# Kernel tuning notes

Measured on AMD Instinct MI355X. Metric: run time of the kernel, lower is better.

## Reference

```python
import jax, jax.numpy as jnp
import numpy as np

B, N, L, H, D, IN = 512, 128, 10, 16, 8, 16
NT = B * N
E = NT * 16

def _lin(key, fan_in, shape):
    b = 1.0 / np.sqrt(fan_in)
    return jax.random.uniform(key, shape, jnp.float32, -b, b)

def setup_inputs() -> dict:
    key = jax.random.key(0)
    ks = jax.random.split(key, 12)
    x = jax.random.normal(ks[0], (NT, IN), jnp.float32)
    # within-graph random edges so to_dense_adj is well defined
    g = jax.random.randint(ks[1], (E,), 0, B)
    i = jax.random.randint(ks[2], (E,), 0, N)
    j = jax.random.randint(ks[3], (E,), 0, N)
    edge_index = jnp.stack([g * N + i, g * N + j]).astype(jnp.int32)
    return dict(
        x=x,
        gin_w1=_lin(ks[4], H, (2, L, H, H)),   # [ld/ud, layer, H, H]
        gin_b1=_lin(ks[5], H, (2, L, H)),
        gin_w2=_lin(ks[6], H, (2, L, H, H)),
        gin_b2=_lin(ks[7], H, (2, L, H)),
        mean_w=_lin(ks[8], H, (2, H, D)),
        mean_b=jnp.zeros((2, D), jnp.float32),
        std_w=_lin(ks[9], H, (2, H, D)),
        std_b=jnp.zeros((2, D), jnp.float32),
        edge_index=edge_index,
    )

def _encoder(x, w1, b1, w2, b2, mw, mb, sw, sb, src, dst):
    # PyG GIN stack: GINConv(MLP[Lin->ReLU->Lin]), eps=0, sum aggregation,
    # ReLU between layers (dropout = identity in eval mode).
    h = x
    for l in range(L):
        agg = jax.ops.segment_sum(h[src], dst, num_segments=NT)
        t = h + agg  # (1+eps)*x + sum_{j in N(i)} x_j with eps=0
        t = jnp.maximum(t @ w1[l] + b1[l], 0.0) @ w2[l] + b2[l]
        h = jnp.maximum(t, 0.0) if l < L - 1 else t
    mean = h @ mw + mb
    std = jax.nn.softplus(h @ sw + sb)
    return mean, std

def reference(x, gin_w1, gin_b1, gin_w2, gin_b2, mean_w, mean_b, std_w, std_b, edge_index):
    src, dst = edge_index[0], edge_index[1]
    enc = jax.vmap(_encoder, in_axes=(None, 0, 0, 0, 0, 0, 0, 0, 0, None, None))
    mean, std = enc(x, gin_w1, gin_b1, gin_w2, gin_b2,
                    mean_w, mean_b, std_w, std_b, src, dst)  # [2, NT, D]
    # reparameterized sample: eps ~ N(0,1) (prior.sample, detached)
    eps = jax.random.normal(jax.random.key(42), (2, NT, D), jnp.float32)
    z = mean + std * eps
    z_ld = z[0].reshape(B, N, D)
    z_ud = z[1].reshape(B, N, D)
    logits = jnp.einsum('bnd,bmd->bnm', z_ld, z_ud)  # per-graph inner-product decode
    dense_adj = jnp.zeros((B, N, N), jnp.float32).at[src // N, src % N, dst % N].add(1.0)
    n_pos = dense_adj.sum()
    posw = (B * N * N - n_pos) / n_pos
    # BCE-with-logits, pos_weight, reduction='sum'
    nll = jnp.sum(posw * dense_adj * jax.nn.softplus(-logits)
                  + (1.0 - dense_adj) * jax.nn.softplus(logits))
    # KL(N(mean,std) || N(0,1)), summed over both encoders
    kl = jnp.sum(-jnp.log(std) + 0.5 * (std * std + mean * mean) - 0.5)
    return nll, kl, jax.nn.sigmoid(logits), dense_adj
```

## Files before the change

kernel.cpp:

```cpp
#include <hip/hip_runtime.h>

#define B_    512
#define N_    128
#define L_    10
#define H_    16
#define D_    8
#define NT_   65536
#define E_    1048576
#define NNB_  8388608
#define CAP_  4096
#define CCAP_ 2816
#define HS_   20

__device__ __forceinline__ unsigned rotl32(unsigned v, int r){ return (v<<r)|(v>>(32-r)); }

__device__ __forceinline__ void threefry2x32(unsigned c0, unsigned c1, unsigned &o0, unsigned &o1){
  const unsigned ks0 = 0u, ks1 = 42u, ks2 = 0u ^ 42u ^ 0x1BD11BDAu;
  unsigned x0 = c0 + ks0, x1 = c1 + ks1;
#define TFR(r) { x0 += x1; x1 = rotl32(x1, r); x1 ^= x0; }
  TFR(13) TFR(15) TFR(26) TFR(6)   x0 += ks1; x1 += ks2 + 1u;
  TFR(17) TFR(29) TFR(16) TFR(24)  x0 += ks2; x1 += ks0 + 2u;
  TFR(13) TFR(15) TFR(26) TFR(6)   x0 += ks0; x1 += ks1 + 3u;
  TFR(17) TFR(29) TFR(16) TFR(24)  x0 += ks1; x1 += ks2 + 4u;
  TFR(13) TFR(15) TFR(26) TFR(6)   x0 += ks2; x1 += ks0 + 5u;
#undef TFR
  o0 = x0; o1 = x1;
}

__device__ __forceinline__ float erfinv_f(float x){
  float w = -log1pf(-x*x);
  float p;
  if (w < 5.0f) {
    w -= 2.5f;
    p = 2.81022636e-08f;
    p = fmaf(p, w, 3.43273939e-07f);
    p = fmaf(p, w, -3.5233877e-06f);
    p = fmaf(p, w, -4.39150654e-06f);
    p = fmaf(p, w, 0.00021858087f);
    p = fmaf(p, w, -0.00125372503f);
    p = fmaf(p, w, -0.00417768164f);
    p = fmaf(p, w, 0.246640727f);
    p = fmaf(p, w, 1.50140941f);
  } else {
    w = sqrtf(w) - 3.0f;
    p = -0.000200214257f;
    p = fmaf(p, w, 0.000100950558f);
    p = fmaf(p, w, 0.00134934322f);
    p = fmaf(p, w, -0.00367342844f);
    p = fmaf(p, w, 0.00573950773f);
    p = fmaf(p, w, -0.0076224613f);
    p = fmaf(p, w, 0.00943887047f);
    p = fmaf(p, w, 1.00167406f);
    p = fmaf(p, w, 2.83297682f);
  }
  return p * x;
}

__device__ __forceinline__ float softplus_f(float x){
  return fmaxf(x, 0.0f) + log1pf(expf(-fabsf(x)));
}

__device__ __forceinline__ void blockReduceAdd(double v, double* target){
  __shared__ double red[4];
  int lane = threadIdx.x & 63;
  int w    = threadIdx.x >> 6;
  #pragma unroll
  for(int off = 32; off > 0; off >>= 1) v += __shfl_down(v, off);
  if(lane == 0) red[w] = v;
  __syncthreads();
  if(threadIdx.x == 0){
    double s = red[0];
    int nw = (blockDim.x + 63) >> 6;
    for(int k = 1; k < nw; k++) s += red[k];
    atomicAdd(target, s);
  }
}

__global__ __launch_bounds__(256)
void k_bin(const int* __restrict__ ei, int* __restrict__ gcount,
           unsigned short* __restrict__ ebuf){
  __shared__ int cnt[512];
  __shared__ int gb[512];
  const int t = threadIdx.x;
  cnt[t] = 0; cnt[t + 256] = 0;
  __syncthreads();
  int kv[8];
  const int base = blockIdx.x * 2048;
  #pragma unroll
  for(int q = 0; q < 8; q++){
    int e = base + q*256 + t;
    int s = ei[e];
    int d = ei[E_ + e];
    int g = d >> 7;
    kv[q] = (g << 14) | ((s & 127) << 7) | (d & 127);
    atomicAdd(&cnt[g], 1);
  }
  __syncthreads();
  #pragma unroll
  for(int g = 0; g < 512; g += 256){
    int c = cnt[g + t];
    gb[g + t] = c ? atomicAdd(&gcount[g + t], c) : 0;
    cnt[g + t] = 0;
  }
  __syncthreads();
  #pragma unroll
  for(int q = 0; q < 8; q++){
    int g = kv[q] >> 14;
    int pos = atomicAdd(&cnt[g], 1);
    int idx = gb[g] + pos;
    if(idx < CAP_) ebuf[(size_t)g*CAP_ + idx] = (unsigned short)(kv[q] & 0x3FFF);
  }
}

__global__ __launch_bounds__(128)
void k_csr(const unsigned short* __restrict__ ebuf, const int* __restrict__ gcount,
           unsigned short* __restrict__ gcol, int* __restrict__ grow){
  __shared__ int cnt[128], off[128], sc[128];
  const int b = blockIdx.x, t = threadIdx.x;
  int ec = gcount[b]; if(ec > CAP_) ec = CAP_;
  const unsigned short* eb = ebuf + (size_t)b*CAP_;
  cnt[t] = 0;
  __syncthreads();
  for(int q = t; q < ec; q += 128) atomicAdd(&cnt[eb[q] & 127], 1);
  __syncthreads();
  int pdeg = (cnt[t] + 3) & ~3;
  sc[t] = pdeg;
  __syncthreads();
  for(int o = 1; o < 128; o <<= 1){
    int v = (t >= o) ? sc[t - o] : 0;
    __syncthreads();
    sc[t] += v;
    __syncthreads();
  }
  off[t] = sc[t] - pdeg;
  grow[b*129 + t] = off[t];
  if(t == 127) grow[b*129 + 128] = sc[127];
  cnt[t] = 0;
  __syncthreads();
  {
    uint4 s128; s128.x = s128.y = s128.z = s128.w = 0x00800080u;
    uint4* g4 = (uint4*)(gcol + (size_t)b*CCAP_);
    #pragma unroll
    for(int k = 0; k < 3; k++){ int q = t + 128*k; if(q < CCAP_/8) g4[q] = s128; }
  }
  __syncthreads();
  for(int q = t; q < ec; q += 128){
    int pk = eb[q];
    int d = pk & 127;
    int pos = atomicAdd(&cnt[d], 1);
    int idx = off[d] + pos;
    if(idx < CCAP_) gcol[(size_t)b*CCAP_ + idx] = (unsigned short)(pk >> 7);
  }
}

__global__ __launch_bounds__(256, 4)
void k_mega(const float* __restrict__ x, const unsigned short* __restrict__ gcol,
            const int* __restrict__ grow,
            const float* __restrict__ gw1, const float* __restrict__ gb1,
            const float* __restrict__ gw2, const float* __restrict__ gb2,
            const float* __restrict__ mw,  const float* __restrict__ mb,
            const float* __restrict__ sw,  const float* __restrict__ sb,
            float* __restrict__ z, double* acc){
  __shared__ __align__(16) float hh[2][129*HS_ + 4];
  __shared__ __align__(16) unsigned short col_l[CCAP_];
  const int b = blockIdx.x, e = blockIdx.y, t = threadIdx.x;
  const int i = t >> 1, p = t & 1;

  {
    const float4* x4 = (const float4*)x + (size_t)b*512;
    #pragma unroll
    for(int k = 0; k < 2; k++){
      int q = t + 256*k;
      float4 v = x4[q];
      *(float4*)&hh[0][(q >> 2)*HS_ + (q & 3)*4] = v;
    }
    if(t < 16){ hh[0][128*HS_ + t] = 0.0f; hh[1][128*HS_ + t] = 0.0f; }
  }
  {
    const uint4* gc4 = (const uint4*)(gcol + (size_t)b*CCAP_);
    uint4* cl4 = (uint4*)col_l;
    #pragma unroll
    for(int k = 0; k < 2; k++){ int q = t + 256*k; if(q < CCAP_/8) cl4[q] = gc4[q]; }
  }
  const int r0 = grow[b*129 + i], r1 = grow[b*129 + i + 1];
  __syncthreads();

  const float* w1g = gw1 + e*(L_*256);
  const float* w2g = gw2 + e*(L_*256);
  const float* b1g = gb1 + e*(L_*16);
  const float* b2g = gb2 + e*(L_*16);

  for(int l = 0; l < L_; l++){
    const float* hb = hh[l & 1];
    float*       hn = hh[(l + 1) & 1];
    float a[8];
    {
      const float4* hp = (const float4*)&hb[i*HS_ + p*8];
      float4 s0 = hp[0], s1 = hp[1];
      a[0]=s0.x; a[1]=s0.y; a[2]=s0.z; a[3]=s0.w;
      a[4]=s1.x; a[5]=s1.y; a[6]=s1.z; a[7]=s1.w;
    }
    for(int r = r0; r < r1; r += 4){
      ushort4 c4 = *(const ushort4*)&col_l[r];
      const float4* n0 = (const float4*)&hb[c4.x*HS_ + p*8];
      const float4* n1 = (const float4*)&hb[c4.y*HS_ + p*8];
      const float4* n2 = (const float4*)&hb[c4.z*HS_ + p*8];
      const float4* n3 = (const float4*)&hb[c4.w*HS_ + p*8];
      #pragma unroll
      for(int c = 0; c < 2; c++){
        float4 v0 = n0[c], v1 = n1[c], v2 = n2[c], v3 = n3[c];
        a[c*4+0] += v0.x + v1.x + v2.x + v3.x;
        a[c*4+1] += v0.y + v1.y + v2.y + v3.y;
        a[c*4+2] += v0.z + v1.z + v2.z + v3.z;
        a[c*4+3] += v0.w + v1.w + v2.w + v3.w;
      }
    }
    float ag[16];
    #pragma unroll
    for(int q = 0; q < 8; q++){
      float o = __shfl_xor(a[q], 1);
      ag[q]     = p ? o    : a[q];
      ag[q + 8] = p ? a[q] : o;
    }
    float u[16];
    #pragma unroll
    for(int j = 0; j < 16; j++){
      float s = b1g[l*16 + j];
      #pragma unroll
      for(int k = 0; k < 16; k++) s = fmaf(ag[k], w1g[l*256 + k*16 + j], s);
      u[j] = fmaxf(s, 0.0f);
    }
    float ov[16];
    #pragma unroll
    for(int c = 0; c < 16; c++){
      float s = b2g[l*16 + c];
      #pragma unroll
      for(int k = 0; k < 16; k++) s = fmaf(u[k], w2g[l*256 + k*16 + c], s);
      ov[c] = (l < L_-1) ? fmaxf(s, 0.0f) : s;
    }
    {
      float4* hw = (float4*)&hn[i*HS_ + p*8];
      hw[0] = make_float4(p ? ov[8]  : ov[0], p ? ov[9]  : ov[1],
                          p ? ov[10] : ov[2], p ? ov[11] : ov[3]);
      hw[1] = make_float4(p ? ov[12] : ov[4], p ? ov[13] : ov[5],
                          p ? ov[14] : ov[6], p ? ov[15] : ov[7]);
    }
    __syncthreads();
  }

  float hv[16];
  {
    const float4* hp = (const float4*)&hh[0][i*HS_];
    float4 a0 = hp[0], a1 = hp[1], a2 = hp[2], a3 = hp[3];
    hv[0]=a0.x; hv[1]=a0.y; hv[2]=a0.z; hv[3]=a0.w;
    hv[4]=a1.x; hv[5]=a1.y; hv[6]=a1.z; hv[7]=a1.w;
    hv[8]=a2.x; hv[9]=a2.y; hv[10]=a2.z; hv[11]=a2.w;
    hv[12]=a3.x; hv[13]=a3.y; hv[14]=a3.z; hv[15]=a3.w;
  }
  const float* mwg = mw + e*128 + p*4; const float* mbg = mb + e*8 + p*4;
  const float* swg = sw + e*128 + p*4; const float* sbg = sb + e*8 + p*4;
  double kll = 0.0;
  float zv[4];
  unsigned fbase = ((unsigned)e*NT_ + (unsigned)(b*128 + i))*8u + (unsigned)(p*4);
  float mmv[4], ssv[4];
  {
    float4 m4 = *(const float4*)mbg;
    float4 s4 = *(const float4*)sbg;
    mmv[0]=m4.x; mmv[1]=m4.y; mmv[2]=m4.z; mmv[3]=m4.w;
    ssv[0]=s4.x; ssv[1]=s4.y; ssv[2]=s4.z; ssv[3]=s4.w;
    #pragma unroll
    for(int k = 0; k < 16; k++){
      float4 mw4 = *(const float4*)(mwg + k*8);
      float4 sw4 = *(const float4*)(swg + k*8);
      float hk = hv[k];
      mmv[0]=fmaf(hk, mw4.x, mmv[0]); mmv[1]=fmaf(hk, mw4.y, mmv[1]);
      mmv[2]=fmaf(hk, mw4.z, mmv[2]); mmv[3]=fmaf(hk, mw4.w, mmv[3]);
      ssv[0]=fmaf(hk, sw4.x, ssv[0]); ssv[1]=fmaf(hk, sw4.y, ssv[1]);
      ssv[2]=fmaf(hk, sw4.z, ssv[2]); ssv[3]=fmaf(hk, sw4.w, ssv[3]);
    }
  }
  #pragma unroll
  for(int dd = 0; dd < 4; dd++){
    float mm = mmv[dd], ss = ssv[dd];
    float stdv = softplus_f(ss);
    unsigned o0, o1; threefry2x32(0u, fbase + dd, o0, o1);
    unsigned bits = o0 ^ o1;
    float uu = __uint_as_float((bits >> 9) | 0x3f800000u) - 1.0f;
    const float lo = -0.99999994f;
    float uval = fmaxf(lo, fmaf(uu, 2.0f, lo));
    float eps = 1.41421356f * erfinv_f(uval);
    zv[dd] = mm + stdv * eps;
    float stdc = fmaxf(stdv, 1e-37f);
    float term = 0.5f*(stdv*stdv + mm*mm) - logf(stdc) - 0.5f;
    if(!(term == term) || term > 1e30f) term = 1e30f;
    kll += (double)term;
  }
  {
    float4* zp = (float4*)(z + (size_t)fbase);
    zp[0] = make_float4(zv[0], zv[1], zv[2], zv[3]);
  }
  blockReduceAdd(kll, acc + 1);
}

#define TSB_ 132
__global__ __launch_bounds__(256, 4)
void k_decode(const float* __restrict__ z, const unsigned short* __restrict__ ebuf,
              const int* __restrict__ gcount, float* __restrict__ sig,
              float* __restrict__ adj, double* acc){
  __shared__ float zl[512];
  __shared__ float zu[1152];
  __shared__ unsigned tile32[64*TSB_/4];
  const int b = blockIdx.x >> 1, h = blockIdx.x & 1, t = threadIdx.x;
  const float* zld = z + (size_t)b*1024 + h*512;
  const float* zud = z + (size_t)NT_*8 + (size_t)b*1024;
  for(int k = t; k < 1024; k += 256){
    if(k < 512) zl[k] = zld[k];
    zu[(k >> 3)*9 + (k & 7)] = zud[k];
  }
  {
    uint4 zz; zz.x = zz.y = zz.z = zz.w = 0u;
    uint4* t4 = (uint4*)tile32;
    for(int k = t; k < 64*TSB_/16; k += 256) t4[k] = zz;
  }
  __syncthreads();
  {
    int ec = gcount[b]; if(ec > CAP_) ec = CAP_;
    const unsigned short* eb = ebuf + (size_t)b*CAP_;
    for(int q = t; q < ec; q += 256){
      int pk = eb[q];
      int src = pk >> 7;
      if((src >> 6) == h){
        int cell = (src & 63)*TSB_ + (pk & 127);
        atomicAdd(&tile32[cell >> 2], 1u << ((cell & 3)*8));
      }
    }
  }
  __syncthreads();
  double local = 0.0;
  float* sigb = sig + (size_t)b*16384 + h*8192;
  float* adjb = adj + (size_t)b*16384 + h*8192;
  for(int it = 0; it < 8; it++){
    int base = it*1024 + t*4;
    int n = base >> 7, mcol = base & 127;
    const float* za = &zl[n*8];
    float xs[4];
    #pragma unroll
    for(int c = 0; c < 4; c++){
      const float* zb = &zu[(mcol + c)*9];
      float xx = 0.0f;
      #pragma unroll
      for(int d = 0; d < 8; d++) xx = fmaf(za[d], zb[d], xx);
      xs[c] = xx;
    }
    unsigned packed = tile32[(n*TSB_ + mcol) >> 2];
    float4 av;
    av.x = (float)( packed        & 0xFF);
    av.y = (float)((packed >> 8)  & 0xFF);
    av.z = (float)((packed >> 16) & 0xFF);
    av.w = (float)((packed >> 24) & 0xFF);
    float ads[4] = {av.x, av.y, av.z, av.w};
    float sgs[4];
    #pragma unroll
    for(int c = 0; c < 4; c++){
      float xx = xs[c];
      sgs[c] = 1.0f / (1.0f + expf(-xx));
      float cc  = log1pf(expf(-fabsf(xx)));
      float spp = fmaxf(xx, 0.0f) + cc;
      float spn = fmaxf(-xx, 0.0f) + cc;
      local += (double)(7.0f*ads[c]*spn + (1.0f - ads[c])*spp);
    }
    ((float4*)(sigb + base))[0] = make_float4(sgs[0], sgs[1], sgs[2], sgs[3]);
    ((float4*)(adjb + base))[0] = av;
  }
  blockReduceAdd(local, acc + 0);
}

__device__ __forceinline__ float clamp_finite(double v){
  if(v != v) return 0.0f;
  if(v >  3.3e38) return  3.3e38f;
  if(v < -3.3e38) return -3.3e38f;
  return (float)v;
}
__global__ void k_final(const double* __restrict__ acc, float* __restrict__ out){
  if(threadIdx.x == 0){
    out[0] = clamp_finite(acc[0]);
    out[1] = clamp_finite(acc[1]);
  }
}

extern "C" void kernel_launch(void* const* d_in, const int* in_sizes, int n_in,
                              void* d_out, int out_size, void* d_ws, size_t ws_size,
                              hipStream_t stream){
  const float* x   = (const float*)d_in[0];
  const float* gw1 = (const float*)d_in[1];
  const float* gb1 = (const float*)d_in[2];
  const float* gw2 = (const float*)d_in[3];
  const float* gb2 = (const float*)d_in[4];
  const float* mw  = (const float*)d_in[5];
  const float* mb  = (const float*)d_in[6];
  const float* sw  = (const float*)d_in[7];
  const float* sb  = (const float*)d_in[8];
  const int*   ei  = (const int*)d_in[9];

  float* out = (float*)d_out;
  float* sig = out + 2;
  float* adj = out + 2 + NNB_;

  char* ws = (char*)d_ws;
  int*            gcount = (int*)(ws);
  double*         acc    = (double*)(ws + 2048);
  unsigned short* ebuf   = (unsigned short*)(ws + 4096);
  unsigned short* gcol   = (unsigned short*)(ws + 4096 + 2*512*CAP_);
  int*            grow   = (int*)(ws + 4096 + 2*512*CAP_ + 2*512*CCAP_);
  float*          z      = (float*)(ws + 4096 + 2*512*CAP_ + 2*512*CCAP_ + 4*512*132);

  hipMemsetAsync(ws, 0, 4096, stream);

  k_bin   <<<E_/2048, 256, 0, stream>>>(ei, gcount, ebuf);
  k_csr   <<<B_, 128, 0, stream>>>(ebuf, gcount, gcol, grow);
  k_mega  <<<dim3(B_, 2), 256, 0, stream>>>(x, gcol, grow, gw1, gb1, gw2, gb2,
                                            mw, mb, sw, sb, z, acc);
  k_decode<<<B_*2, 256, 0, stream>>>(z, ebuf, gcount, sig, adj, acc);
  k_final <<<1, 64, 0, stream>>>(acc, out);
}
```

Before: 256.3 us.

## Keep per-column decode operand in registers and compute full mean/std per thread

```diff
diff --git a/kernel.cpp b/kernel.cpp
--- a/kernel.cpp
+++ b/kernel.cpp
@@ -257,31 +257,26 @@
     hv[8]=a2.x; hv[9]=a2.y; hv[10]=a2.z; hv[11]=a2.w;
     hv[12]=a3.x; hv[13]=a3.y; hv[14]=a3.z; hv[15]=a3.w;
   }
-  const float* mwg = mw + e*128 + p*4; const float* mbg = mb + e*8 + p*4;
-  const float* swg = sw + e*128 + p*4; const float* sbg = sb + e*8 + p*4;
+  const float* mwg = mw + e*128; const float* mbg = mb + e*8;
+  const float* swg = sw + e*128; const float* sbg = sb + e*8;
+  float md[8], sd[8];
+  #pragma unroll
+  for(int d = 0; d < 8; d++){
+    float mm = mbg[d], ss = sbg[d];
+    #pragma unroll
+    for(int k = 0; k < 16; k++){
+      mm = fmaf(hv[k], mwg[k*8 + d], mm);
+      ss = fmaf(hv[k], swg[k*8 + d], ss);
+    }
+    md[d] = mm; sd[d] = ss;
+  }
   double kll = 0.0;
   float zv[4];
   unsigned fbase = ((unsigned)e*NT_ + (unsigned)(b*128 + i))*8u + (unsigned)(p*4);
-  float mmv[4], ssv[4];
-  {
-    float4 m4 = *(const float4*)mbg;
-    float4 s4 = *(const float4*)sbg;
-    mmv[0]=m4.x; mmv[1]=m4.y; mmv[2]=m4.z; mmv[3]=m4.w;
-    ssv[0]=s4.x; ssv[1]=s4.y; ssv[2]=s4.z; ssv[3]=s4.w;
-    #pragma unroll
-    for(int k = 0; k < 16; k++){
-      float4 mw4 = *(const float4*)(mwg + k*8);
-      float4 sw4 = *(const float4*)(swg + k*8);
-      float hk = hv[k];
-      mmv[0]=fmaf(hk, mw4.x, mmv[0]); mmv[1]=fmaf(hk, mw4.y, mmv[1]);
-      mmv[2]=fmaf(hk, mw4.z, mmv[2]); mmv[3]=fmaf(hk, mw4.w, mmv[3]);
-      ssv[0]=fmaf(hk, sw4.x, ssv[0]); ssv[1]=fmaf(hk, sw4.y, ssv[1]);
-      ssv[2]=fmaf(hk, sw4.z, ssv[2]); ssv[3]=fmaf(hk, sw4.w, ssv[3]);
-    }
-  }
   #pragma unroll
   for(int dd = 0; dd < 4; dd++){
-    float mm = mmv[dd], ss = ssv[dd];
+    float mm = p ? md[4+dd] : md[dd];
+    float ss = p ? sd[4+dd] : sd[dd];
     float stdv = softplus_f(ss);
     unsigned o0, o1; threefry2x32(0u, fbase + dd, o0, o1);
     unsigned bits = o0 ^ o1;
@@ -308,19 +303,23 @@
               const int* __restrict__ gcount, float* __restrict__ sig,
               float* __restrict__ adj, double* acc){
   __shared__ float zl[512];
-  __shared__ float zu[1152];
   __shared__ unsigned tile32[64*TSB_/4];
   const int b = blockIdx.x >> 1, h = blockIdx.x & 1, t = threadIdx.x;
+  const int col = t & 127, rg = t >> 7;
   const float* zld = z + (size_t)b*1024 + h*512;
-  const float* zud = z + (size_t)NT_*8 + (size_t)b*1024;
-  for(int k = t; k < 1024; k += 256){
-    if(k < 512) zl[k] = zld[k];
-    zu[(k >> 3)*9 + (k & 7)] = zud[k];
-  }
+  #pragma unroll
+  for(int k = 0; k < 2; k++) zl[t + 256*k] = zld[t + 256*k];
   {
     uint4 zz; zz.x = zz.y = zz.z = zz.w = 0u;
     uint4* t4 = (uint4*)tile32;
     for(int k = t; k < 64*TSB_/16; k += 256) t4[k] = zz;
+  }
+  float zb[8];
+  {
+    const float4* zu4 = (const float4*)(z + (size_t)NT_*8 + (size_t)b*1024 + col*8);
+    float4 u0 = zu4[0], u1 = zu4[1];
+    zb[0]=u0.x; zb[1]=u0.y; zb[2]=u0.z; zb[3]=u0.w;
+    zb[4]=u1.x; zb[5]=u1.y; zb[6]=u1.z; zb[7]=u1.w;
   }
   __syncthreads();
   {
@@ -339,38 +338,21 @@
   double local = 0.0;
   float* sigb = sig + (size_t)b*16384 + h*8192;
   float* adjb = adj + (size_t)b*16384 + h*8192;
-  for(int it = 0; it < 8; it++){
-    int base = it*1024 + t*4;
-    int n = base >> 7, mcol = base & 127;
-    const float* za = &zl[n*8];
-    float xs[4];
-    #pragma unroll
-    for(int c = 0; c < 4; c++){
-      const float* zb = &zu[(mcol + c)*9];
-      float xx = 0.0f;
-      #pragma unroll
-      for(int d = 0; d < 8; d++) xx = fmaf(za[d], zb[d], xx);
-      xs[c] = xx;
-    }
-    unsigned packed = tile32[(n*TSB_ + mcol) >> 2];
-    float4 av;
-    av.x = (float)( packed        & 0xFF);
-    av.y = (float)((packed >> 8)  & 0xFF);
-    av.z = (float)((packed >> 16) & 0xFF);
-    av.w = (float)((packed >> 24) & 0xFF);
-    float ads[4] = {av.x, av.y, av.z, av.w};
-    float sgs[4];
-    #pragma unroll
-    for(int c = 0; c < 4; c++){
-      float xx = xs[c];
-      sgs[c] = 1.0f / (1.0f + expf(-xx));
-      float cc  = log1pf(expf(-fabsf(xx)));
-      float spp = fmaxf(xx, 0.0f) + cc;
-      float spn = fmaxf(-xx, 0.0f) + cc;
-      local += (double)(7.0f*ads[c]*spn + (1.0f - ads[c])*spp);
-    }
-    ((float4*)(sigb + base))[0] = make_float4(sgs[0], sgs[1], sgs[2], sgs[3]);
-    ((float4*)(adjb + base))[0] = av;
+  for(int r = 0; r < 32; r++){
+    int n = rg*32 + r;
+    float4 a0 = *(const float4*)&zl[n*8];
+    float4 a1 = *(const float4*)&zl[n*8 + 4];
+    float xx = a0.x*zb[0] + a0.y*zb[1] + a0.z*zb[2] + a0.w*zb[3]
+             + a1.x*zb[4] + a1.y*zb[5] + a1.z*zb[6] + a1.w*zb[7];
+    unsigned packed = tile32[(n*TSB_ + col) >> 2];
+    float ad = (float)((packed >> ((col & 3)*8)) & 0xFF);
+    float sg = 1.0f / (1.0f + expf(-xx));
+    float cc  = log1pf(expf(-fabsf(xx)));
+    float spp = fmaxf(xx, 0.0f) + cc;
+    float spn = fmaxf(-xx, 0.0f) + cc;
+    local += (double)(7.0f*ad*spn + (1.0f - ad)*spp);
+    sigb[n*128 + col] = sg;
+    adjb[n*128 + col] = ad;
   }
   blockReduceAdd(local, acc + 0);
 }
```

Result: faster. 250.7 us (-2.2%).
